# Kernel tuning notes

Hardware: AMD Instinct MI355X
Metric: run time of the kernel (lower is better)

Reference implementation:

```python
import jax, jax.numpy as jnp
from jax import lax
import numpy as np

V, EMB, UNITS, NL = 32000, 256, 256, 2
B, T = 64, 256


def setup_inputs() -> dict:
    key = jax.random.key(0)
    ks = jax.random.split(key, 9)
    seqs = jax.random.randint(ks[0], (B, T), 1, V)
    # ragged padding at the end (token 0 is the pad/mask token)
    lengths = jax.random.randint(ks[1], (B,), T // 2, T + 1)
    seqs = jnp.where(jnp.arange(T)[None, :] < lengths[:, None], seqs, 0)
    s = 0.05
    E = jax.random.normal(ks[2], (V, EMB), jnp.float32) * 0.001
    Wf = jax.random.normal(ks[3], (NL, UNITS, 4 * UNITS), jnp.float32) * s
    Uf = jax.random.normal(ks[4], (NL, UNITS, 4 * UNITS), jnp.float32) * s
    bf = jnp.zeros((NL, 4 * UNITS), jnp.float32)
    Wb = jax.random.normal(ks[5], (NL, UNITS, 4 * UNITS), jnp.float32) * s
    Ub = jax.random.normal(ks[6], (NL, UNITS, 4 * UNITS), jnp.float32) * s
    bb = jnp.zeros((NL, 4 * UNITS), jnp.float32)
    return {"seqs": seqs, "E": E, "Wf": Wf, "Uf": Uf, "bf": bf,
            "Wb": Wb, "Ub": Ub, "bb": bb}


def lstm_scan(x, mask, W, U, b):
    """Keras LSTM with masking: masked steps carry h,c (output = carried h).
    x: [B,Tm,D], mask: [B,Tm] bool. Gate order i,f,g,o. Returns [B,Tm,U]."""
    Bd = x.shape[0]
    Ud = U.shape[0]
    # precompute input projections for all timesteps (one big GEMM)
    zx = jnp.einsum('btd,dk->btk', x, W) + b  # [B,Tm,4U]

    def step(carry, inp):
        h, c = carry
        zxt, mt = inp  # [B,4U], [B]
        z = zxt + h @ U
        i, f, g, o = jnp.split(z, 4, axis=-1)
        c_new = jax.nn.sigmoid(f) * c + jax.nn.sigmoid(i) * jnp.tanh(g)
        h_new = jax.nn.sigmoid(o) * jnp.tanh(c_new)
        m = mt[:, None]
        h2 = jnp.where(m, h_new, h)
        c2 = jnp.where(m, c_new, c)
        return (h2, c2), h2

    h0 = jnp.zeros((Bd, Ud), x.dtype)
    (_, _), hs = lax.scan(step, (h0, h0),
                          (jnp.swapaxes(zx, 0, 1), jnp.swapaxes(mask, 0, 1)))
    return jnp.swapaxes(hs, 0, 1)


def reference(seqs, E, Wf, Uf, bf, Wb, Ub, bb):
    mask = seqs != 0                      # mask_zero=True
    emb = E[seqs]                         # [B,T,EMB]
    fm, bm = mask[:, :-1], mask[:, 1:]
    fxs = [emb[:, :-1]]
    bxs = [emb[:, 1:]]
    for l in range(NL):
        fxs.append(lstm_scan(fxs[-1], fm, Wf[l], Uf[l], bf[l]))
        # go_backwards=True: process reversed input/mask, then tf.reverse back
        bx_rev = lstm_scan(bxs[-1][:, ::-1], bm[:, ::-1], Wb[l], Ub[l], bb[l])
        bxs.append(bx_rev[:, ::-1])
    # stack fxs[0..NL] then bxs[0..NL]: [2*(NL+1), B, T-1, UNITS]
    return jnp.stack(fxs + bxs)
```

## Files before the change

### kernel.cpp

```cpp
#include <hip/hip_runtime.h>
#include <hip/hip_bf16.h>


#define TT 256
#define TM 255
#define NU 256
#define NG 1024
#define BB 64

typedef __attribute__((ext_vector_type(8))) short short8;
typedef __attribute__((ext_vector_type(4))) float f32x4;
typedef __attribute__((ext_vector_type(4))) unsigned int u32x4;

__device__ __forceinline__ unsigned short f2bf(float v) {
  unsigned int x = __float_as_uint(v);
  return (unsigned short)((x + 0x7FFFu + ((x >> 16) & 1u)) >> 16);
}
__device__ __forceinline__ float sigm(float x) { return 1.f / (1.f + __expf(-x)); }
__device__ __forceinline__ float tanhp(float x) {
  x = fminf(fmaxf(x, -15.f), 15.f);
  float e = __expf(-2.f * x);
  return (1.f - e) / (1.f + e);
}
#define VMCNT(n) asm volatile("s_waitcnt vmcnt(" #n ")" ::: "memory")
#define LGKM0() asm volatile("s_waitcnt lgkmcnt(0)" ::: "memory")
#define SCHEDBAR() __builtin_amdgcn_sched_barrier(0)
#define BAR() __builtin_amdgcn_s_barrier()

#define LLC_LOAD16(dst, ptr) \
  asm volatile("global_load_dwordx4 %0, %1, off sc0 sc1" : "=&v"(dst) : "v"(ptr) : "memory")
#define CACH_LOAD16(dst, ptr) \
  asm volatile("global_load_dwordx4 %0, %1, off" : "=&v"(dst) : "v"(ptr) : "memory")
#define STORE4(ptr, val) \
  asm volatile("global_store_dword %0, %1, off" :: "v"(ptr), "v"(val) : "memory")

__global__ void embed_kernel(const int* __restrict__ seqs, const float* __restrict__ E,
                             unsigned short* __restrict__ embb, float* __restrict__ out) {
  int b = blockIdx.x, t = blockIdx.y, d = threadIdx.x;
  int s = seqs[b * TT + t];
  float v = E[(size_t)s * NU + d];
  embb[((size_t)(b * TT + t)) * NU + d] = f2bf(v);
  if (t < TM) out[(((size_t)(0 * BB + b)) * TM + t) * NU + d] = v;
  if (t >= 1) out[(((size_t)(3 * BB + b)) * TM + (t - 1)) * NU + d] = v;
}

__launch_bounds__(512, 1)
__global__ void lstm_kernel(const int* __restrict__ seqs,
                            const float* __restrict__ Wf, const float* __restrict__ Uf,
                            const float* __restrict__ bf,
                            const float* __restrict__ Wb, const float* __restrict__ Ub,
                            const float* __restrict__ bb,
                            const unsigned short* __restrict__ embb,
                            unsigned int* __restrict__ Hbuf, float* __restrict__ out) {
  extern __shared__ char smem[];
  float* zpart = (float*)smem;
  char* hlb0 = smem + 16384;
  char* hlb1 = smem + 24576;
  unsigned char* mskl = (unsigned char*)(smem + 32768);

  const int tid = threadIdx.x;
  const int blk = blockIdx.x;
  const int cluster = blk & 7, slice = blk >> 3;
  const int dir = cluster >> 2, rg = cluster & 3;
  const int ubase = slice << 4;
  const int wave = tid >> 6, g = wave & 3, kh = wave >> 2;
  const int lane = tid & 63, q = lane >> 4, n15 = lane & 15;
  const int tlay = tid >> 8, ct = tid & 255, crow = ct >> 4, cn = ct & 15;
  const int brow = rg * 16 + crow;

  const float* W0 = dir ? Wb : Wf;
  const float* U0 = dir ? Ub : Uf;
  const float* b0p = dir ? bb : bf;
  const float* mats[4] = {W0, U0, W0 + NU * NG, U0 + NU * NG};

  short8 wreg[16];
  {
    const int col = g * 256 + ubase + n15;
    #pragma unroll
    for (int m = 0; m < 4; m++) {
      #pragma unroll
      for (int kb = 0; kb < 4; kb++) {
        short8 t;
        #pragma unroll
        for (int j = 0; j < 8; j++)
          t[j] = (short)f2bf(mats[m][(size_t)(kh * 128 + kb * 32 + q * 8 + j) * NG + col]);
        wreg[m * 4 + kb] = t;
      }
    }
  }

  for (int i = tid; i < 64 * 256; i += 512) {
    int row = i >> 8, s = i & 255;
    mskl[i] = (s < TM) ? (seqs[row * TT + (dir ? TM - s : s)] != 0) : 0;
  }

  float bi[4];
  {
    const float* bp = tlay ? (b0p + NG) : b0p;
    #pragma unroll
    for (int gg = 0; gg < 4; gg++) bi[gg] = bp[(gg << 8) + ubase + cn];
  }
  float cst = 0.f, hv = 0.f;

  __syncthreads();

  const int wsw = (tid * 16) ^ (((tid >> 5) & 7) << 4);
  const int fb = n15 * 512 + kh * 256;
  const int fx = (n15 & 7) << 4;
  const int zwr = (g << 9) + (kh << 8) + n15;

  unsigned int* hst = Hbuf + ((size_t)(tlay * 16 + cluster)) * 4096 + crow * 256 + ubase + cn;
  float* dump = (float*)((char*)Hbuf + 524288) + (blk * 512 + tid);

  const float* pendA = dump;
  float pendV = 0.f;
  bool havePend = false;

  short8 ea[4];

  {
    int tx = dir ? TM : 0;
    const unsigned short* ep =
        embb + ((size_t)((rg * 16 + n15) * TT + tx)) * NU + kh * 128 + q * 8;
    f32x4 acc0 = {0.f, 0.f, 0.f, 0.f};
    #pragma unroll
    for (int kb = 0; kb < 4; kb++) {
      short8 a = *(const short8*)(ep + kb * 32);
      acc0 = __builtin_amdgcn_mfma_f32_16x16x32_bf16(a, wreg[kb], acc0, 0, 0, 0);
    }
    #pragma unroll
    for (int j = 0; j < 4; j++) zpart[zwr + (((q << 2) + j) << 4)] = acc0[j];
    LGKM0(); SCHEDBAR(); BAR();
    if (tlay == 0) {
      float z[4];
      #pragma unroll
      for (int gg = 0; gg < 4; gg++)
        z[gg] = zpart[(gg * 2) * 256 + crow * 16 + cn] +
                zpart[(gg * 2 + 1) * 256 + crow * 16 + cn] + bi[gg];
      float cnw = sigm(z[1]) * cst + sigm(z[0]) * tanhp(z[2]);
      float hnw = sigm(z[3]) * tanhp(cnw);
      if (mskl[brow * 256 + 0]) { cst = cnw; hv = hnw; }
      int tout = dir ? TM - 1 : 0;
      pendA = out + (((size_t)((1 + dir * 3) * BB + brow)) * TM + tout) * NU + ubase + cn;
      pendV = hv;
    }
    havePend = true;
    {
      int tx1 = dir ? TM - 1 : 1;
      const unsigned short* e1 =
          embb + ((size_t)((rg * 16 + n15) * TT + tx1)) * NU + kh * 128 + q * 8;
      #pragma unroll
      for (int kb = 0; kb < 4; kb++) CACH_LOAD16(ea[kb], e1 + kb * 32);
    }
    SCHEDBAR();
    __hip_atomic_store(hst, (1u << 16) | (unsigned)f2bf(hv),
                       __ATOMIC_RELAXED, __HIP_MEMORY_SCOPE_AGENT);
  }

  for (int tau = 1; tau < 256; ++tau) {
    const bool doL0 = (tau < TM);
    const bool doH1 = (tau >= 2);
    const int step = tlay ? tau - 1 : tau;

    VMCNT(1); SCHEDBAR();

    f32x4 acc0 = {0.f, 0.f, 0.f, 0.f}, acc1 = {0.f, 0.f, 0.f, 0.f};
    if (doL0) {
      #pragma unroll
      for (int kb = 0; kb < 4; kb++)
        acc0 = __builtin_amdgcn_mfma_f32_16x16x32_bf16(ea[kb], wreg[kb], acc0, 0, 0, 0);
      SCHEDBAR();
    }

    const unsigned tg = (unsigned)tau;
    const int p = (tau + 1) & 1;
    const unsigned int* c0a = Hbuf + ((size_t)(p * 8 + cluster)) * 4096 + tid * 8;
    const unsigned int* c0b = c0a + 4;
    const unsigned int* c1a = Hbuf + ((size_t)((2 + p) * 8 + cluster)) * 4096 + tid * 8;
    const unsigned int* c1b = c1a + 4;
    u32x4 a0 = {0, 0, 0, 0}, a1 = {0, 0, 0, 0}, b0v = {0, 0, 0, 0}, b1v = {0, 0, 0, 0};
    bool first = true;
    int miss = 0;
    for (;;) {
      LLC_LOAD16(a0, c0a);
      LLC_LOAD16(a1, c0b);
      if (doH1) { LLC_LOAD16(b0v, c1a); LLC_LOAD16(b1v, c1b); }
      if (first) {
        if (havePend) { STORE4(pendA, pendV); havePend = false; }
        first = false;
        VMCNT(1);
      } else {
        VMCNT(0);
      }
      SCHEDBAR();
      bool ok = (a0[0] >> 16) == tg && (a0[1] >> 16) == tg && (a0[2] >> 16) == tg &&
                (a0[3] >> 16) == tg && (a1[0] >> 16) == tg && (a1[1] >> 16) == tg &&
                (a1[2] >> 16) == tg && (a1[3] >> 16) == tg;
      if (doH1)
        ok = ok && (b0v[0] >> 16) == tg && (b0v[1] >> 16) == tg && (b0v[2] >> 16) == tg &&
             (b0v[3] >> 16) == tg && (b1v[0] >> 16) == tg && (b1v[1] >> 16) == tg &&
             (b1v[2] >> 16) == tg && (b1v[3] >> 16) == tg;
      if (__all(ok)) break;
      if (++miss > 2) __builtin_amdgcn_s_sleep(1);
    }
    u32x4 s0, s1;
    s0[0] = (a0[0] & 0xFFFFu) | (a0[1] << 16);
    s0[1] = (a0[2] & 0xFFFFu) | (a0[3] << 16);
    s0[2] = (a1[0] & 0xFFFFu) | (a1[1] << 16);
    s0[3] = (a1[2] & 0xFFFFu) | (a1[3] << 16);
    *(u32x4*)(hlb0 + wsw) = s0;
    if (doH1) {
      s1[0] = (b0v[0] & 0xFFFFu) | (b0v[1] << 16);
      s1[1] = (b0v[2] & 0xFFFFu) | (b0v[3] << 16);
      s1[2] = (b1v[0] & 0xFFFFu) | (b1v[1] << 16);
      s1[3] = (b1v[2] & 0xFFFFu) | (b1v[3] << 16);
      *(u32x4*)(hlb1 + wsw) = s1;
    }
    LGKM0(); SCHEDBAR(); BAR();

    #pragma unroll
    for (int kb = 0; kb < 4; kb++) {
      short8 h0f = *(const short8*)(hlb0 + ((fb + kb * 64 + q * 16) ^ fx));
      if (doL0) acc0 = __builtin_amdgcn_mfma_f32_16x16x32_bf16(h0f, wreg[4 + kb], acc0, 0, 0, 0);
      acc1 = __builtin_amdgcn_mfma_f32_16x16x32_bf16(h0f, wreg[8 + kb], acc1, 0, 0, 0);
    }
    if (doH1) {
      #pragma unroll
      for (int kb = 0; kb < 4; kb++) {
        short8 h1f = *(const short8*)(hlb1 + ((fb + kb * 64 + q * 16) ^ fx));
        acc1 = __builtin_amdgcn_mfma_f32_16x16x32_bf16(h1f, wreg[12 + kb], acc1, 0, 0, 0);
      }
    }

    if (doL0) {
      #pragma unroll
      for (int j = 0; j < 4; j++) zpart[zwr + (((q << 2) + j) << 4)] = acc0[j];
    }
    #pragma unroll
    for (int j = 0; j < 4; j++) zpart[2048 + zwr + (((q << 2) + j) << 4)] = acc1[j];
    LGKM0(); SCHEDBAR(); BAR();

    if (tau < TM - 1) {
      int tx1 = dir ? TM - (tau + 1) : (tau + 1);
      const unsigned short* e1 =
          embb + ((size_t)((rg * 16 + n15) * TT + tx1)) * NU + kh * 128 + q * 8;
      #pragma unroll
      for (int kb = 0; kb < 4; kb++) CACH_LOAD16(ea[kb], e1 + kb * 32);
    }
    SCHEDBAR();

    if (tlay ? true : doL0) {
      float z[4];
      #pragma unroll
      for (int gg = 0; gg < 4; gg++)
        z[gg] = zpart[(tlay * 8 + gg * 2) * 256 + crow * 16 + cn] +
                zpart[(tlay * 8 + gg * 2 + 1) * 256 + crow * 16 + cn] + bi[gg];
      float cnw = sigm(z[1]) * cst + sigm(z[0]) * tanhp(z[2]);
      float hnw = sigm(z[3]) * tanhp(cnw);
      if (mskl[brow * 256 + step]) { cst = cnw; hv = hnw; }
      __hip_atomic_store(hst + (size_t)(tau & 1) * 32768,
                         ((unsigned)(tau + 1) << 16) | (unsigned)f2bf(hv),
                         __ATOMIC_RELAXED, __HIP_MEMORY_SCOPE_AGENT);
      int tout = dir ? TM - 1 - step : step;
      pendA = out + (((size_t)((1 + tlay + dir * 3) * BB + brow)) * TM + tout) * NU + ubase + cn;
      pendV = hv;
      havePend = true;
    }
  }

  if (havePend) STORE4(pendA, pendV);
}

extern "C" void kernel_launch(void* const* d_in, const int* in_sizes, int n_in,
                              void* d_out, int out_size, void* d_ws, size_t ws_size,
                              hipStream_t stream) {
  const int* seqs = (const int*)d_in[0];
  const float* E = (const float*)d_in[1];
  const float* Wf = (const float*)d_in[2];
  const float* Uf = (const float*)d_in[3];
  const float* bfp = (const float*)d_in[4];
  const float* Wb = (const float*)d_in[5];
  const float* Ub = (const float*)d_in[6];
  const float* bbp = (const float*)d_in[7];
  float* out = (float*)d_out;

  char* ws = (char*)d_ws;
  unsigned int* Hbuf = (unsigned int*)ws;
  unsigned short* embb = (unsigned short*)(ws + 1048576);

  hipMemsetAsync(Hbuf, 0, 4 * 8 * 4096 * sizeof(unsigned int), stream);

  hipLaunchKernelGGL(embed_kernel, dim3(BB, TT), dim3(256), 0, stream,
                     seqs, E, embb, out);

  int smem = 49152;
  hipFuncSetAttribute(reinterpret_cast<const void*>(lstm_kernel),
                      hipFuncAttributeMaxDynamicSharedMemorySize, smem);
  hipLaunchKernelGGL(lstm_kernel, dim3(128), dim3(512), smem, stream,
                     seqs, Wf, Uf, bfp, Wb, Ub, bbp, embb, Hbuf, out);
}
```

Before: 618.6 us.

## Halve LSTM workgroups by giving each block 32 units instead of 16

Each workgroup now handles two 16-unit column tiles, so it keeps twice the weight registers and issues twice the MFMAs. The grid shrinks from 128 to 64 blocks. Fewer blocks take part in the per-timestep global flag handshake, which should cut synchronisation contention and polling traffic. The cost is double the per-block compute and register pressure (32 short8 weight fragments), which may lengthen the critical path of each step.

```diff
diff --git a/kernel.cpp b/kernel.cpp
--- a/kernel.cpp
+++ b/kernel.cpp
@@ -54,15 +54,15 @@
                             unsigned int* __restrict__ Hbuf, float* __restrict__ out) {
   extern __shared__ char smem[];
   float* zpart = (float*)smem;
-  char* hlb0 = smem + 16384;
-  char* hlb1 = smem + 24576;
-  unsigned char* mskl = (unsigned char*)(smem + 32768);
+  char* hlb0 = smem + 32768;
+  char* hlb1 = smem + 40960;
+  unsigned char* mskl = (unsigned char*)(smem + 49152);
 
   const int tid = threadIdx.x;
   const int blk = blockIdx.x;
   const int cluster = blk & 7, slice = blk >> 3;
   const int dir = cluster >> 2, rg = cluster & 3;
-  const int ubase = slice << 4;
+  const int ubase = slice << 5;
   const int wave = tid >> 6, g = wave & 3, kh = wave >> 2;
   const int lane = tid & 63, q = lane >> 4, n15 = lane & 15;
   const int tlay = tid >> 8, ct = tid & 255, crow = ct >> 4, cn = ct & 15;
@@ -73,18 +73,21 @@
   const float* b0p = dir ? bb : bf;
   const float* mats[4] = {W0, U0, W0 + NU * NG, U0 + NU * NG};
 
-  short8 wreg[16];
+  short8 wreg[32];
   {
-    const int col = g * 256 + ubase + n15;
     #pragma unroll
     for (int m = 0; m < 4; m++) {
       #pragma unroll
       for (int kb = 0; kb < 4; kb++) {
-        short8 t;
         #pragma unroll
-        for (int j = 0; j < 8; j++)
-          t[j] = (short)f2bf(mats[m][(size_t)(kh * 128 + kb * 32 + q * 8 + j) * NG + col]);
-        wreg[m * 4 + kb] = t;
+        for (int nt = 0; nt < 2; nt++) {
+          const int col = g * 256 + ubase + nt * 16 + n15;
+          short8 t;
+          #pragma unroll
+          for (int j = 0; j < 8; j++)
+            t[j] = (short)f2bf(mats[m][(size_t)(kh * 128 + kb * 32 + q * 8 + j) * NG + col]);
+          wreg[(m * 4 + kb) * 2 + nt] = t;
+        }
       }
     }
   }
@@ -94,26 +97,29 @@
     mskl[i] = (s < TM) ? (seqs[row * TT + (dir ? TM - s : s)] != 0) : 0;
   }
 
-  float bi[4];
+  float biA[4], biB[4];
   {
     const float* bp = tlay ? (b0p + NG) : b0p;
     #pragma unroll
-    for (int gg = 0; gg < 4; gg++) bi[gg] = bp[(gg << 8) + ubase + cn];
-  }
-  float cst = 0.f, hv = 0.f;
+    for (int gg = 0; gg < 4; gg++) {
+      biA[gg] = bp[(gg << 8) + ubase + cn];
+      biB[gg] = bp[(gg << 8) + ubase + cn + 16];
+    }
+  }
+  float cstA = 0.f, hvA = 0.f, cstB = 0.f, hvB = 0.f;
 
   __syncthreads();
 
   const int wsw = (tid * 16) ^ (((tid >> 5) & 7) << 4);
   const int fb = n15 * 512 + kh * 256;
   const int fx = (n15 & 7) << 4;
-  const int zwr = (g << 9) + (kh << 8) + n15;
-
-  unsigned int* hst = Hbuf + ((size_t)(tlay * 16 + cluster)) * 4096 + crow * 256 + ubase + cn;
-  float* dump = (float*)((char*)Hbuf + 524288) + (blk * 512 + tid);
-
-  const float* pendA = dump;
-  float pendV = 0.f;
+  unsigned int* hstA = Hbuf + ((size_t)(tlay * 16 + cluster)) * 4096 + crow * 256 + ubase + cn;
+  unsigned int* hstB = hstA + 16;
+  float* dump = (float*)((char*)Hbuf + 524288) + (size_t)(blk * 512 + tid) * 2;
+
+  const float* pendAA = dump;
+  const float* pendAB = dump + 1;
+  float pendVA = 0.f, pendVB = 0.f;
   bool havePend = false;
 
   short8 ea[4];
@@ -122,27 +128,37 @@
     int tx = dir ? TM : 0;
     const unsigned short* ep =
         embb + ((size_t)((rg * 16 + n15) * TT + tx)) * NU + kh * 128 + q * 8;
-    f32x4 acc0 = {0.f, 0.f, 0.f, 0.f};
+    f32x4 accN0 = {0.f, 0.f, 0.f, 0.f}, accN1 = {0.f, 0.f, 0.f, 0.f};
     #pragma unroll
     for (int kb = 0; kb < 4; kb++) {
       short8 a = *(const short8*)(ep + kb * 32);
-      acc0 = __builtin_amdgcn_mfma_f32_16x16x32_bf16(a, wreg[kb], acc0, 0, 0, 0);
-    }
-    #pragma unroll
-    for (int j = 0; j < 4; j++) zpart[zwr + (((q << 2) + j) << 4)] = acc0[j];
+      accN0 = __builtin_amdgcn_mfma_f32_16x16x32_bf16(a, wreg[kb * 2 + 0], accN0, 0, 0, 0);
+      accN1 = __builtin_amdgcn_mfma_f32_16x16x32_bf16(a, wreg[kb * 2 + 1], accN1, 0, 0, 0);
+    }
+    #pragma unroll
+    for (int j = 0; j < 4; j++) {
+      zpart[(g * 4 + kh * 2 + 0) * 256 + (((q << 2) + j) << 4) + n15] = accN0[j];
+      zpart[(g * 4 + kh * 2 + 1) * 256 + (((q << 2) + j) << 4) + n15] = accN1[j];
+    }
     LGKM0(); SCHEDBAR(); BAR();
     if (tlay == 0) {
-      float z[4];
-      #pragma unroll
-      for (int gg = 0; gg < 4; gg++)
-        z[gg] = zpart[(gg * 2) * 256 + crow * 16 + cn] +
-                zpart[(gg * 2 + 1) * 256 + crow * 16 + cn] + bi[gg];
-      float cnw = sigm(z[1]) * cst + sigm(z[0]) * tanhp(z[2]);
-      float hnw = sigm(z[3]) * tanhp(cnw);
-      if (mskl[brow * 256 + 0]) { cst = cnw; hv = hnw; }
+      float zA[4], zB[4];
+      #pragma unroll
+      for (int gg = 0; gg < 4; gg++) {
+        zA[gg] = zpart[(gg * 4 + 0) * 256 + crow * 16 + cn] +
+                 zpart[(gg * 4 + 2) * 256 + crow * 16 + cn] + biA[gg];
+        zB[gg] = zpart[(gg * 4 + 1) * 256 + crow * 16 + cn] +
+                 zpart[(gg * 4 + 3) * 256 + crow * 16 + cn] + biB[gg];
+      }
+      float cA = sigm(zA[1]) * cstA + sigm(zA[0]) * tanhp(zA[2]);
+      float hA = sigm(zA[3]) * tanhp(cA);
+      float cB = sigm(zB[1]) * cstB + sigm(zB[0]) * tanhp(zB[2]);
+      float hB = sigm(zB[3]) * tanhp(cB);
+      if (mskl[brow * 256 + 0]) { cstA = cA; hvA = hA; cstB = cB; hvB = hB; }
       int tout = dir ? TM - 1 : 0;
-      pendA = out + (((size_t)((1 + dir * 3) * BB + brow)) * TM + tout) * NU + ubase + cn;
-      pendV = hv;
+      pendAA = out + (((size_t)((1 + dir * 3) * BB + brow)) * TM + tout) * NU + ubase + cn;
+      pendAB = pendAA + 16;
+      pendVA = hvA; pendVB = hvB;
     }
     havePend = true;
     {
@@ -153,7 +169,9 @@
       for (int kb = 0; kb < 4; kb++) CACH_LOAD16(ea[kb], e1 + kb * 32);
     }
     SCHEDBAR();
-    __hip_atomic_store(hst, (1u << 16) | (unsigned)f2bf(hv),
+    __hip_atomic_store(hstA, (1u << 16) | (unsigned)f2bf(hvA),
+                       __ATOMIC_RELAXED, __HIP_MEMORY_SCOPE_AGENT);
+    __hip_atomic_store(hstB, (1u << 16) | (unsigned)f2bf(hvB),
                        __ATOMIC_RELAXED, __HIP_MEMORY_SCOPE_AGENT);
   }
 
@@ -162,13 +180,16 @@
     const bool doH1 = (tau >= 2);
     const int step = tlay ? tau - 1 : tau;
 
-    VMCNT(1); SCHEDBAR();
-
-    f32x4 acc0 = {0.f, 0.f, 0.f, 0.f}, acc1 = {0.f, 0.f, 0.f, 0.f};
+    VMCNT(2); SCHEDBAR();
+
+    f32x4 a0N0 = {0.f, 0.f, 0.f, 0.f}, a0N1 = {0.f, 0.f, 0.f, 0.f};
+    f32x4 a1N0 = {0.f, 0.f, 0.f, 0.f}, a1N1 = {0.f, 0.f, 0.f, 0.f};
     if (doL0) {
       #pragma unroll
-      for (int kb = 0; kb < 4; kb++)
-        acc0 = __builtin_amdgcn_mfma_f32_16x16x32_bf16(ea[kb], wreg[kb], acc0, 0, 0, 0);
+      for (int kb = 0; kb < 4; kb++) {
+        a0N0 = __builtin_amdgcn_mfma_f32_16x16x32_bf16(ea[kb], wreg[kb * 2 + 0], a0N0, 0, 0, 0);
+        a0N1 = __builtin_amdgcn_mfma_f32_16x16x32_bf16(ea[kb], wreg[kb * 2 + 1], a0N1, 0, 0, 0);
+      }
       SCHEDBAR();
     }
 
@@ -186,9 +207,9 @@
       LLC_LOAD16(a1, c0b);
       if (doH1) { LLC_LOAD16(b0v, c1a); LLC_LOAD16(b1v, c1b); }
       if (first) {
-        if (havePend) { STORE4(pendA, pendV); havePend = false; }
+        if (havePend) { STORE4(pendAA, pendVA); STORE4(pendAB, pendVB); havePend = false; }
         first = false;
-        VMCNT(1);
+        VMCNT(2);
       } else {
         VMCNT(0);
       }
@@ -221,23 +242,34 @@
     #pragma unroll
     for (int kb = 0; kb < 4; kb++) {
       short8 h0f = *(const short8*)(hlb0 + ((fb + kb * 64 + q * 16) ^ fx));
-      if (doL0) acc0 = __builtin_amdgcn_mfma_f32_16x16x32_bf16(h0f, wreg[4 + kb], acc0, 0, 0, 0);
-      acc1 = __builtin_amdgcn_mfma_f32_16x16x32_bf16(h0f, wreg[8 + kb], acc1, 0, 0, 0);
+      if (doL0) {
+        a0N0 = __builtin_amdgcn_mfma_f32_16x16x32_bf16(h0f, wreg[(4 + kb) * 2 + 0], a0N0, 0, 0, 0);
+        a0N1 = __builtin_amdgcn_mfma_f32_16x16x32_bf16(h0f, wreg[(4 + kb) * 2 + 1], a0N1, 0, 0, 0);
+      }
+      a1N0 = __builtin_amdgcn_mfma_f32_16x16x32_bf16(h0f, wreg[(8 + kb) * 2 + 0], a1N0, 0, 0, 0);
+      a1N1 = __builtin_amdgcn_mfma_f32_16x16x32_bf16(h0f, wreg[(8 + kb) * 2 + 1], a1N1, 0, 0, 0);
     }
     if (doH1) {
       #pragma unroll
       for (int kb = 0; kb < 4; kb++) {
         short8 h1f = *(const short8*)(hlb1 + ((fb + kb * 64 + q * 16) ^ fx));
-        acc1 = __builtin_amdgcn_mfma_f32_16x16x32_bf16(h1f, wreg[12 + kb], acc1, 0, 0, 0);
+        a1N0 = __builtin_amdgcn_mfma_f32_16x16x32_bf16(h1f, wreg[(12 + kb) * 2 + 0], a1N0, 0, 0, 0);
+        a1N1 = __builtin_amdgcn_mfma_f32_16x16x32_bf16(h1f, wreg[(12 + kb) * 2 + 1], a1N1, 0, 0, 0);
       }
     }
 
     if (doL0) {
       #pragma unroll
-      for (int j = 0; j < 4; j++) zpart[zwr + (((q << 2) + j) << 4)] = acc0[j];
-    }
-    #pragma unroll
-    for (int j = 0; j < 4; j++) zpart[2048 + zwr + (((q << 2) + j) << 4)] = acc1[j];
+      for (int j = 0; j < 4; j++) {
+        zpart[(g * 4 + kh * 2 + 0) * 256 + (((q << 2) + j) << 4) + n15] = a0N0[j];
+        zpart[(g * 4 + kh * 2 + 1) * 256 + (((q << 2) + j) << 4) + n15] = a0N1[j];
+      }
+    }
+    #pragma unroll
+    for (int j = 0; j < 4; j++) {
+      zpart[4096 + (g * 4 + kh * 2 + 0) * 256 + (((q << 2) + j) << 4) + n15] = a1N0[j];
+      zpart[4096 + (g * 4 + kh * 2 + 1) * 256 + (((q << 2) + j) << 4) + n15] = a1N1[j];
+    }
     LGKM0(); SCHEDBAR(); BAR();
 
     if (tau < TM - 1) {
@@ -250,25 +282,34 @@
     SCHEDBAR();
 
     if (tlay ? true : doL0) {
-      float z[4];
-      #pragma unroll
-      for (int gg = 0; gg < 4; gg++)
-        z[gg] = zpart[(tlay * 8 + gg * 2) * 256 + crow * 16 + cn] +
-                zpart[(tlay * 8 + gg * 2 + 1) * 256 + crow * 16 + cn] + bi[gg];
-      float cnw = sigm(z[1]) * cst + sigm(z[0]) * tanhp(z[2]);
-      float hnw = sigm(z[3]) * tanhp(cnw);
-      if (mskl[brow * 256 + step]) { cst = cnw; hv = hnw; }
-      __hip_atomic_store(hst + (size_t)(tau & 1) * 32768,
-                         ((unsigned)(tau + 1) << 16) | (unsigned)f2bf(hv),
+      float zA[4], zB[4];
+      #pragma unroll
+      for (int gg = 0; gg < 4; gg++) {
+        zA[gg] = zpart[tlay * 4096 + (gg * 4 + 0) * 256 + crow * 16 + cn] +
+                 zpart[tlay * 4096 + (gg * 4 + 2) * 256 + crow * 16 + cn] + biA[gg];
+        zB[gg] = zpart[tlay * 4096 + (gg * 4 + 1) * 256 + crow * 16 + cn] +
+                 zpart[tlay * 4096 + (gg * 4 + 3) * 256 + crow * 16 + cn] + biB[gg];
+      }
+      float cA = sigm(zA[1]) * cstA + sigm(zA[0]) * tanhp(zA[2]);
+      float hA = sigm(zA[3]) * tanhp(cA);
+      float cB = sigm(zB[1]) * cstB + sigm(zB[0]) * tanhp(zB[2]);
+      float hB = sigm(zB[3]) * tanhp(cB);
+      if (mskl[brow * 256 + step]) { cstA = cA; hvA = hA; cstB = cB; hvB = hB; }
+      unsigned twA = ((unsigned)(tau + 1) << 16) | (unsigned)f2bf(hvA);
+      unsigned twB = ((unsigned)(tau + 1) << 16) | (unsigned)f2bf(hvB);
+      __hip_atomic_store(hstA + (size_t)(tau & 1) * 32768, twA,
+                         __ATOMIC_RELAXED, __HIP_MEMORY_SCOPE_AGENT);
+      __hip_atomic_store(hstB + (size_t)(tau & 1) * 32768, twB,
                          __ATOMIC_RELAXED, __HIP_MEMORY_SCOPE_AGENT);
       int tout = dir ? TM - 1 - step : step;
-      pendA = out + (((size_t)((1 + tlay + dir * 3) * BB + brow)) * TM + tout) * NU + ubase + cn;
-      pendV = hv;
+      pendAA = out + (((size_t)((1 + tlay + dir * 3) * BB + brow)) * TM + tout) * NU + ubase + cn;
+      pendAB = pendAA + 16;
+      pendVA = hvA; pendVB = hvB;
       havePend = true;
     }
   }
 
-  if (havePend) STORE4(pendA, pendV);
+  if (havePend) { STORE4(pendAA, pendVA); STORE4(pendAB, pendVB); }
 }
 
 extern "C" void kernel_launch(void* const* d_in, const int* in_sizes, int n_in,
@@ -293,9 +334,9 @@
   hipLaunchKernelGGL(embed_kernel, dim3(BB, TT), dim3(256), 0, stream,
                      seqs, E, embb, out);
 
-  int smem = 49152;
+  int smem = 65536;
   hipFuncSetAttribute(reinterpret_cast<const void*>(lstm_kernel),
                       hipFuncAttributeMaxDynamicSharedMemorySize, smem);
-  hipLaunchKernelGGL(lstm_kernel, dim3(128), dim3(512), smem, stream,
+  hipLaunchKernelGGL(lstm_kernel, dim3(64), dim3(512), smem, stream,
                      seqs, Wf, Uf, bfp, Wb, Ub, bbp, embb, Hbuf, out);
 }
```

Measured after the change: 949.4 us. 53.5% more time.

## Split per-step wavefront into layer-0 then layer-1 phases to shorten critical path

Applied to the files above, without the earlier changes.

Each timestep is restructured into two phases. Layer 0 first waits only for its own h, computes and publishes its new state, and only then does layer 1 wait for its input h and compute. Publishing layer-0 h earlier shortens the cross-block dependency chain so other clusters can start their next step sooner. In exchange each step has extra barriers and a second polling loop, and the zpart buffer is shared between the phases, which shrinks LDS use.

```diff
diff --git a/kernel.cpp b/kernel.cpp
--- a/kernel.cpp
+++ b/kernel.cpp
@@ -42,6 +42,12 @@
   embb[((size_t)(b * TT + t)) * NU + d] = f2bf(v);
   if (t < TM) out[(((size_t)(0 * BB + b)) * TM + t) * NU + d] = v;
   if (t >= 1) out[(((size_t)(3 * BB + b)) * TM + (t - 1)) * NU + d] = v;
+}
+
+__device__ __forceinline__ bool tags8(const u32x4& x, const u32x4& y, unsigned tg) {
+  return (x[0] >> 16) == tg && (x[1] >> 16) == tg && (x[2] >> 16) == tg &&
+         (x[3] >> 16) == tg && (y[0] >> 16) == tg && (y[1] >> 16) == tg &&
+         (y[2] >> 16) == tg && (y[3] >> 16) == tg;
 }
 
 __launch_bounds__(512, 1)
@@ -54,9 +60,9 @@
                             unsigned int* __restrict__ Hbuf, float* __restrict__ out) {
   extern __shared__ char smem[];
   float* zpart = (float*)smem;
-  char* hlb0 = smem + 16384;
-  char* hlb1 = smem + 24576;
-  unsigned char* mskl = (unsigned char*)(smem + 32768);
+  char* hlb0 = smem + 8192;
+  char* hlb1 = smem + 16384;
+  unsigned char* mskl = (unsigned char*)(smem + 24576);
 
   const int tid = threadIdx.x;
   const int blk = blockIdx.x;
@@ -114,7 +120,6 @@
 
   const float* pendA = dump;
   float pendV = 0.f;
-  bool havePend = false;
 
   short8 ea[4];
 
@@ -141,10 +146,8 @@
       float hnw = sigm(z[3]) * tanhp(cnw);
       if (mskl[brow * 256 + 0]) { cst = cnw; hv = hnw; }
       int tout = dir ? TM - 1 : 0;
-      pendA = out + (((size_t)((1 + dir * 3) * BB + brow)) * TM + tout) * NU + ubase + cn;
-      pendV = hv;
-    }
-    havePend = true;
+      STORE4(out + (((size_t)((1 + dir * 3) * BB + brow)) * TM + tout) * NU + ubase + cn, hv);
+    }
     {
       int tx1 = dir ? TM - 1 : 1;
       const unsigned short* e1 =
@@ -159,10 +162,11 @@
 
   for (int tau = 1; tau < 256; ++tau) {
     const bool doL0 = (tau < TM);
-    const bool doH1 = (tau >= 2);
-    const int step = tlay ? tau - 1 : tau;
-
-    VMCNT(1); SCHEDBAR();
+    const unsigned tg = (unsigned)tau;
+    const int p = (tau + 1) & 1;
+
+    if (tlay == 0) { VMCNT(0); } else { VMCNT(1); }
+    SCHEDBAR();
 
     f32x4 acc0 = {0.f, 0.f, 0.f, 0.f}, acc1 = {0.f, 0.f, 0.f, 0.f};
     if (doL0) {
@@ -172,74 +176,112 @@
       SCHEDBAR();
     }
 
-    const unsigned tg = (unsigned)tau;
-    const int p = (tau + 1) & 1;
     const unsigned int* c0a = Hbuf + ((size_t)(p * 8 + cluster)) * 4096 + tid * 8;
     const unsigned int* c0b = c0a + 4;
-    const unsigned int* c1a = Hbuf + ((size_t)((2 + p) * 8 + cluster)) * 4096 + tid * 8;
-    const unsigned int* c1b = c1a + 4;
-    u32x4 a0 = {0, 0, 0, 0}, a1 = {0, 0, 0, 0}, b0v = {0, 0, 0, 0}, b1v = {0, 0, 0, 0};
-    bool first = true;
-    int miss = 0;
-    for (;;) {
-      LLC_LOAD16(a0, c0a);
-      LLC_LOAD16(a1, c0b);
-      if (doH1) { LLC_LOAD16(b0v, c1a); LLC_LOAD16(b1v, c1b); }
-      if (first) {
-        if (havePend) { STORE4(pendA, pendV); havePend = false; }
-        first = false;
-        VMCNT(1);
-      } else {
-        VMCNT(0);
+    u32x4 a0 = {0, 0, 0, 0}, a1 = {0, 0, 0, 0};
+    {
+      bool first = true;
+      int miss = 0;
+      for (;;) {
+        LLC_LOAD16(a0, c0a);
+        LLC_LOAD16(a1, c0b);
+        if (first) {
+          first = false;
+          if (tlay == 1) { STORE4(pendA, pendV); VMCNT(1); } else { VMCNT(0); }
+        } else {
+          VMCNT(0);
+        }
+        SCHEDBAR();
+        if (__all(tags8(a0, a1, tg))) break;
+        if (++miss > 2) __builtin_amdgcn_s_sleep(1);
       }
-      SCHEDBAR();
-      bool ok = (a0[0] >> 16) == tg && (a0[1] >> 16) == tg && (a0[2] >> 16) == tg &&
-                (a0[3] >> 16) == tg && (a1[0] >> 16) == tg && (a1[1] >> 16) == tg &&
-                (a1[2] >> 16) == tg && (a1[3] >> 16) == tg;
-      if (doH1)
-        ok = ok && (b0v[0] >> 16) == tg && (b0v[1] >> 16) == tg && (b0v[2] >> 16) == tg &&
-             (b0v[3] >> 16) == tg && (b1v[0] >> 16) == tg && (b1v[1] >> 16) == tg &&
-             (b1v[2] >> 16) == tg && (b1v[3] >> 16) == tg;
-      if (__all(ok)) break;
-      if (++miss > 2) __builtin_amdgcn_s_sleep(1);
-    }
-    u32x4 s0, s1;
+    }
+    u32x4 s0;
     s0[0] = (a0[0] & 0xFFFFu) | (a0[1] << 16);
     s0[1] = (a0[2] & 0xFFFFu) | (a0[3] << 16);
     s0[2] = (a1[0] & 0xFFFFu) | (a1[1] << 16);
     s0[3] = (a1[2] & 0xFFFFu) | (a1[3] << 16);
     *(u32x4*)(hlb0 + wsw) = s0;
-    if (doH1) {
-      s1[0] = (b0v[0] & 0xFFFFu) | (b0v[1] << 16);
-      s1[1] = (b0v[2] & 0xFFFFu) | (b0v[3] << 16);
-      s1[2] = (b1v[0] & 0xFFFFu) | (b1v[1] << 16);
-      s1[3] = (b1v[2] & 0xFFFFu) | (b1v[3] << 16);
-      *(u32x4*)(hlb1 + wsw) = s1;
-    }
+    LGKM0(); SCHEDBAR(); BAR();
+
+    if (doL0) {
+      #pragma unroll
+      for (int kb = 0; kb < 4; kb++) {
+        short8 h0f = *(const short8*)(hlb0 + ((fb + kb * 64 + q * 16) ^ fx));
+        acc0 = __builtin_amdgcn_mfma_f32_16x16x32_bf16(h0f, wreg[4 + kb], acc0, 0, 0, 0);
+      }
+      #pragma unroll
+      for (int j = 0; j < 4; j++) zpart[zwr + (((q << 2) + j) << 4)] = acc0[j];
+    }
+    LGKM0(); SCHEDBAR(); BAR();
+
+    if (tlay == 0 && doL0) {
+      float z[4];
+      #pragma unroll
+      for (int gg = 0; gg < 4; gg++)
+        z[gg] = zpart[(gg * 2) * 256 + crow * 16 + cn] +
+                zpart[(gg * 2 + 1) * 256 + crow * 16 + cn] + bi[gg];
+      float cnw = sigm(z[1]) * cst + sigm(z[0]) * tanhp(z[2]);
+      float hnw = sigm(z[3]) * tanhp(cnw);
+      if (mskl[brow * 256 + tau]) { cst = cnw; hv = hnw; }
+      __hip_atomic_store(hst + (size_t)(tau & 1) * 32768,
+                         ((unsigned)(tau + 1) << 16) | (unsigned)f2bf(hv),
+                         __ATOMIC_RELAXED, __HIP_MEMORY_SCOPE_AGENT);
+      int tout = dir ? TM - 1 - tau : tau;
+      pendA = out + (((size_t)((1 + dir * 3) * BB + brow)) * TM + tout) * NU + ubase + cn;
+      pendV = hv;
+    }
+
+    const unsigned int* c1a = Hbuf + ((size_t)((2 + p) * 8 + cluster)) * 4096 + tid * 8;
+    const unsigned int* c1b = c1a + 4;
+    u32x4 b0v = {0, 0, 0, 0}, b1v = {0, 0, 0, 0};
+    {
+      const bool st = (tlay == 0) && doL0;
+      bool first = true;
+      int miss = 0;
+      for (;;) {
+        LLC_LOAD16(b0v, c1a);
+        LLC_LOAD16(b1v, c1b);
+        if (first) {
+          first = false;
+          if (st) { STORE4(pendA, pendV); VMCNT(1); } else { VMCNT(0); }
+        } else {
+          VMCNT(0);
+        }
+        SCHEDBAR();
+        if (__all(tags8(b0v, b1v, tg))) break;
+        if (++miss > 2) __builtin_amdgcn_s_sleep(1);
+      }
+    }
+    u32x4 s1;
+    s1[0] = (b0v[0] & 0xFFFFu) | (b0v[1] << 16);
+    s1[1] = (b0v[2] & 0xFFFFu) | (b0v[3] << 16);
+    s1[2] = (b1v[0] & 0xFFFFu) | (b1v[1] << 16);
+    s1[3] = (b1v[2] & 0xFFFFu) | (b1v[3] << 16);
+    *(u32x4*)(hlb1 + wsw) = s1;
     LGKM0(); SCHEDBAR(); BAR();
 
     #pragma unroll
     for (int kb = 0; kb < 4; kb++) {
       short8 h0f = *(const short8*)(hlb0 + ((fb + kb * 64 + q * 16) ^ fx));
-      if (doL0) acc0 = __builtin_amdgcn_mfma_f32_16x16x32_bf16(h0f, wreg[4 + kb], acc0, 0, 0, 0);
       acc1 = __builtin_amdgcn_mfma_f32_16x16x32_bf16(h0f, wreg[8 + kb], acc1, 0, 0, 0);
-    }
-    if (doH1) {
-      #pragma unroll
-      for (int kb = 0; kb < 4; kb++) {
-        short8 h1f = *(const short8*)(hlb1 + ((fb + kb * 64 + q * 16) ^ fx));
-        acc1 = __builtin_amdgcn_mfma_f32_16x16x32_bf16(h1f, wreg[12 + kb], acc1, 0, 0, 0);
-      }
-    }
-
-    if (doL0) {
-      #pragma unroll
-      for (int j = 0; j < 4; j++) zpart[zwr + (((q << 2) + j) << 4)] = acc0[j];
-    }
-    #pragma unroll
-    for (int j = 0; j < 4; j++) zpart[2048 + zwr + (((q << 2) + j) << 4)] = acc1[j];
-    LGKM0(); SCHEDBAR(); BAR();
-
+      short8 h1f = *(const short8*)(hlb1 + ((fb + kb * 64 + q * 16) ^ fx));
+      acc1 = __builtin_amdgcn_mfma_f32_16x16x32_bf16(h1f, wreg[12 + kb], acc1, 0, 0, 0);
+    }
+    #pragma unroll
+    for (int j = 0; j < 4; j++) zpart[zwr + (((q << 2) + j) << 4)] = acc1[j];
+    LGKM0(); SCHEDBAR(); BAR();
+
+    if (tlay == 1) {
+      float z[4];
+      #pragma unroll
+      for (int gg = 0; gg < 4; gg++)
+        z[gg] = zpart[(gg * 2) * 256 + crow * 16 + cn] +
+                zpart[(gg * 2 + 1) * 256 + crow * 16 + cn] + bi[gg];
+      float cnw = sigm(z[1]) * cst + sigm(z[0]) * tanhp(z[2]);
+      float hnw = sigm(z[3]) * tanhp(cnw);
+      if (mskl[brow * 256 + (tau - 1)]) { cst = cnw; hv = hnw; }
+    }
     if (tau < TM - 1) {
       int tx1 = dir ? TM - (tau + 1) : (tau + 1);
       const unsigned short* e1 =
@@ -248,27 +290,17 @@
       for (int kb = 0; kb < 4; kb++) CACH_LOAD16(ea[kb], e1 + kb * 32);
     }
     SCHEDBAR();
-
-    if (tlay ? true : doL0) {
-      float z[4];
-      #pragma unroll
-      for (int gg = 0; gg < 4; gg++)
-        z[gg] = zpart[(tlay * 8 + gg * 2) * 256 + crow * 16 + cn] +
-                zpart[(tlay * 8 + gg * 2 + 1) * 256 + crow * 16 + cn] + bi[gg];
-      float cnw = sigm(z[1]) * cst + sigm(z[0]) * tanhp(z[2]);
-      float hnw = sigm(z[3]) * tanhp(cnw);
-      if (mskl[brow * 256 + step]) { cst = cnw; hv = hnw; }
+    if (tlay == 1) {
       __hip_atomic_store(hst + (size_t)(tau & 1) * 32768,
                          ((unsigned)(tau + 1) << 16) | (unsigned)f2bf(hv),
                          __ATOMIC_RELAXED, __HIP_MEMORY_SCOPE_AGENT);
-      int tout = dir ? TM - 1 - step : step;
-      pendA = out + (((size_t)((1 + tlay + dir * 3) * BB + brow)) * TM + tout) * NU + ubase + cn;
+      int tout = dir ? TM - 1 - (tau - 1) : (tau - 1);
+      pendA = out + (((size_t)((2 + dir * 3) * BB + brow)) * TM + tout) * NU + ubase + cn;
       pendV = hv;
-      havePend = true;
-    }
-  }
-
-  if (havePend) STORE4(pendA, pendV);
+    }
+  }
+
+  if (tlay == 1) STORE4(pendA, pendV);
 }
 
 extern "C" void kernel_launch(void* const* d_in, const int* in_sizes, int n_in,
@@ -293,7 +325,7 @@
   hipLaunchKernelGGL(embed_kernel, dim3(BB, TT), dim3(256), 0, stream,
                      seqs, E, embb, out);
 
-  int smem = 49152;
+  int smem = 40960;
   hipFuncSetAttribute(reinterpret_cast<const void*>(lstm_kernel),
                       hipFuncAttributeMaxDynamicSharedMemorySize, smem);
   hipLaunchKernelGGL(lstm_kernel, dim3(128), dim3(512), smem, stream,
```

Result: slower. 761.9 us (+23.2%).
